# Kernel tuning notes

Measured on AMD Instinct MI355X. Metric: run time of the kernel, lower is better.

The kernel has to match this reference:

```python
import jax, jax.numpy as jnp
import numpy as np

PERIOD = 24
NUM_ITERATIONS = 2


def _window_size():
    w = max(3, PERIOD // 2)  # 12
    if w % 2 == 0:
        w += 1  # 13
    return w


def moving_average(s, w):
    # s: [N, L]; replicate-pad by w//2 on each side, then width-w mean conv ('VALID')
    pad = w // 2
    sp = jnp.pad(s, ((0, 0), (pad, pad)), mode='edge')[:, None, :]  # [N,1,L+2*pad]
    k = jnp.ones((1, 1, w), s.dtype) / w
    y = jax.lax.conv_general_dilated(sp, k, window_strides=(1,), padding='VALID',
                                     dimension_numbers=('NCH', 'OIH', 'NCH'))
    return y[:, 0, :]  # [N, L]


def extract_seasonal(d):
    # d: [N, L] with L a multiple of PERIOD. Strided indices i, i+P, ... correspond
    # to reshape [N, C, P] with fixed last axis; median over cycles, broadcast back.
    N, L = d.shape
    C = L // PERIOD
    sub = d.reshape(N, C, PERIOD)
    med = jnp.median(sub, axis=1)  # [N, P] (C=121 is odd -> matches torch.median)
    return jnp.broadcast_to(med[:, None, :], (N, C, PERIOD)).reshape(N, L)


def setup_inputs() -> dict:
    key = jax.random.key(0)
    x = jax.random.normal(key, (64, 2904, 207), dtype=jnp.float32)
    return {"x": x}


def reference(x):
    # x: [B, L, F] -> process all features at once as [B*F, L]
    B, L, F = x.shape
    s = jnp.transpose(x, (0, 2, 1)).reshape(B * F, L)
    w = _window_size()
    trend = moving_average(s, w)
    for _ in range(NUM_ITERATIONS):
        seasonal = extract_seasonal(s - trend)
        trend = moving_average(s - seasonal, w)
    residual = s - trend - seasonal

    def unflatten(a):
        return jnp.transpose(a.reshape(B, F, L), (0, 2, 1))  # [B, L, F]

    return unflatten(trend), unflatten(seasonal), unflatten(residual)
```

## Files before the change

### kernel.cpp

```cpp
#include <hip/hip_runtime.h>

#define LROW    2904
#define PERIOD  24
#define CYC     121
#define NF      207
#define KF      208
#define NB      64
#define NROWS   13248
#define NSLOT   61
#define NT      256
#define LTILE   24
#define NLT     121
#define K2GRID  (NB * NLT)
#define K2CHUNK (K2GRID / 8)
#define R13     (1.f / 13.f)

typedef unsigned short us2 __attribute__((ext_vector_type(2)));

__device__ __forceinline__ int clampi(int i) {
    return i < 0 ? 0 : (i >= LROW ? LROW - 1 : i);
}
__device__ __forceinline__ unsigned quantk(float d) {
    int ki = (int)fmaf(d, 4096.f, 32768.f);
    ki = ki < 0 ? 0 : (ki > 65535 ? 65535 : ki);
    return (unsigned)ki;
}
__device__ __forceinline__ float dqmid(unsigned k) {
    return ((float)(int)k - 32767.5f) * (1.f / 4096.f);
}

__device__ __forceinline__ unsigned selN(const unsigned (&K)[NSLOT], int thr) {
    unsigned T = 0;
    const us2 one2 = __builtin_bit_cast(us2, 0x00010001u);
    for (int bit = 15; bit >= 0; --bit) {
        unsigned Tp = T | (1u << bit);
        unsigned tm32 = (Tp - 1u) | ((Tp - 1u) << 16);
        us2 tm2 = __builtin_bit_cast(us2, tm32);
        us2 acc = __builtin_bit_cast(us2, 0u);
        #pragma unroll
        for (int s = 0; s < NSLOT; ++s) {
            us2 kv = __builtin_bit_cast(us2, K[s]);
            us2 dd = __builtin_elementwise_sub_sat(kv, tm2);
            us2 mm = __builtin_elementwise_min(dd, one2);
            acc = acc + mm;
        }
        unsigned a = __builtin_bit_cast(unsigned, acc);
        int cnt = (int)(a & 0xFFFFu) + (int)(a >> 16);
        if (cnt >= thr) T = Tp;
    }
    return T;
}

__global__ __launch_bounds__(256) void k_keys(const float* __restrict__ x,
                                              unsigned* __restrict__ keys) {
    __shared__ float T[62 * NF];
    const int b  = blockIdx.x;
    const int cp = blockIdx.y;
    const int fl = threadIdx.x;
    const int fe = fl < NF ? fl : NF - 1;
    const int l0 = cp * 48;
    const float* xb = x + (size_t)b * (LROW * NF);
    unsigned* kb = keys + ((size_t)b * PERIOD * NSLOT + cp) * KF + fl;

    if (cp != 0 && cp != 60) {
        const float2* s2 = (const float2*)(xb + (size_t)(l0 - 8) * NF);
        float2* t2 = (float2*)T;
        for (int i = fl; i < 62 * NF / 2; i += NT) t2[i] = s2[i];
    } else {
        for (int i = fl; i < 62 * NF; i += NT) {
            int lr = i / NF, ff = i - lr * NF;
            T[i] = xb[(size_t)clampi(l0 - 8 + lr) * NF + ff];
        }
    }
    __syncthreads();

    float r[13];
    #pragma unroll
    for (int i = 0; i < 13; ++i) r[i] = T[(i + 1) * NF + fe];
    float sum = ((r[0]+r[1])+(r[2]+r[3]))+((r[4]+r[5])+(r[6]+r[7]))
              + ((r[8]+r[9])+(r[10]+r[11])) + r[12];

    if (cp < 60) {
        unsigned pend[PERIOD];
        #pragma unroll
        for (int j = 0; j < 48; ++j) {
            float xn = T[(j + 14) * NF + fe];
            sum += xn - r[0];
            unsigned k = quantk(r[7] - sum * R13);
            if (j < 24) pend[j] = k;
            else if (fl < KF)
                kb[(size_t)(j - 24) * (NSLOT * KF)] = pend[j - 24] | (k << 16);
            #pragma unroll
            for (int i = 0; i < 12; ++i) r[i] = r[i + 1];
            r[12] = xn;
        }
    } else {
        #pragma unroll
        for (int j = 0; j < 24; ++j) {
            float xn = T[(j + 14) * NF + fe];
            sum += xn - r[0];
            unsigned k = quantk(r[7] - sum * R13);
            if (fl < KF)
                kb[(size_t)j * (NSLOT * KF)] = k | 0xFFFF0000u;
            #pragma unroll
            for (int i = 0; i < 12; ++i) r[i] = r[i + 1];
            r[12] = xn;
        }
    }
}

__global__ __launch_bounds__(256) void k_med0(const unsigned* __restrict__ keys,
                                              unsigned short* __restrict__ m0key) {
    const int d  = blockIdx.x;
    const int bp = (d & 7) * 192 + (d >> 3);
    const int fl = threadIdx.x;
    const int fx = fl < KF ? fl : KF - 1;
    unsigned K[NSLOT];
    const unsigned* kp = keys + (size_t)bp * NSLOT * KF + fx;
    #pragma unroll
    for (int s = 0; s < NSLOT; ++s) K[s] = kp[(size_t)s * KF];
    unsigned T = selN(K, 62);
    if (fl < KF) m0key[(size_t)bp * KF + fl] = (unsigned short)T;
}

__global__ __launch_bounds__(256) void k_edge2(const unsigned* __restrict__ keys,
                                               const unsigned short* __restrict__ m0key,
                                               float* __restrict__ medBedge) {
    const int d  = blockIdx.x;
    const int be = (d & 7) * 96 + (d >> 3);
    const int b = be / 12, e = be - 12 * b;
    const int p = (e < 6) ? e : e + 12;
    const int fl = threadIdx.x;
    const int fx = fl < KF ? fl : KF - 1;

    float m0[PERIOD];
    #pragma unroll
    for (int q = 0; q < PERIOD; ++q)
        m0[q] = dqmid(m0key[(size_t)(b * PERIOD + q) * KF + fx]);

    float wph = 0.f, we = 0.f;
    #pragma unroll
    for (int ee = 0; ee < 12; ++ee) if (ee == e) {
        const int pp = (ee < 6) ? ee : ee + 12;
        #pragma unroll
        for (int t = 0; t < 13; ++t) wph += m0[(pp + 18 + t) % 24];
        #pragma unroll
        for (int t = -6; t <= 6; ++t) {
            int aa = pp + t; if (aa < 0) aa = 0; if (aa > 23) aa = 23;
            we += m0[aa];
        }
    }

    unsigned K[NSLOT];
    const unsigned* kp = keys + (size_t)(b * PERIOD + p) * NSLOT * KF + fx;
    #pragma unroll
    for (int s = 0; s < NSLOT; ++s) K[s] = kp[(size_t)s * KF];

    unsigned m = (unsigned)m0key[(size_t)(b * PERIOD + p) * KF + fx];
    unsigned xk = ((p < 6) ? K[0] : K[60]) & 0xFFFFu;
    unsigned y = quantk(dqmid(xk) + (we - wph) * R13);

    int thr = (y > m) ? 61 : 63;
    unsigned v = selN(K, thr);
    bool up = (y > m) && (xk <= m);
    bool dn = (y < m) && (xk >= m);
    unsigned nm = up ? (y < v ? y : v) : (dn ? (y > v ? y : v) : m);
    if (fl < KF)
        medBedge[(size_t)(b * 12 + e) * KF + fl] = dqmid(nm) + wph * R13;
}

__global__ __launch_bounds__(NT, 5) void stl_outputs(const float* __restrict__ x,
                                                     const unsigned short* __restrict__ m0key,
                                                     const float* __restrict__ medBedge,
                                                     float* __restrict__ out) {
    __shared__ float T[(LTILE + 12) * NF];

    const int d   = blockIdx.x;
    const int blk = (d & 7) * K2CHUNK + (d >> 3);
    const int b  = blk / NLT;
    const int kk = blk - b * NLT;
    const int l0 = kk * LTILE;
    const int t  = threadIdx.x;
    const float* xb = x + (size_t)b * (LROW * NF);

    if (kk != 0 && kk != NLT - 1) {
        const float2* s2 = (const float2*)(xb + (size_t)(l0 - 6) * NF);
        float2* t2 = (float2*)T;
        for (int i = t; i < (LTILE + 12) * NF / 2; i += NT) t2[i] = s2[i];
    } else {
        for (int i = t; i < (LTILE + 12) * NF; i += NT) {
            int lr = i / NF;
            int ff = i - lr * NF;
            T[i] = xb[(size_t)clampi(l0 - 6 + lr) * NF + ff];
        }
    }
    __syncthreads();

    if (t < NF) {
        float m0[PERIOD];
        #pragma unroll
        for (int q = 0; q < PERIOD; ++q)
            m0[q] = dqmid(m0key[(size_t)(b * PERIOD + q) * KF + t]);
        float W0[PERIOD];
        {
            float s = 0.f;
            #pragma unroll
            for (int q = 0; q < 13; ++q) s += m0[q];
            W0[0] = s;
            #pragma unroll
            for (int q = 1; q < PERIOD; ++q)
                W0[q] = W0[q - 1] + m0[(q + 12) % 24] - m0[q - 1];
        }
        float lm[PERIOD];
        #pragma unroll
        for (int e = 0; e < 12; ++e) {
            int p = (e < 6) ? e : e + 12;
            lm[p] = medBedge[(size_t)(b * 12 + e) * KF + t];
        }
        #pragma unroll
        for (int p = 6; p < 18; ++p) lm[p] = m0[p] + W0[p - 6] * R13;
        float wt[PERIOD];
        {
            float s = 0.f;
            #pragma unroll
            for (int q = 0; q < 13; ++q) s += lm[q];
            wt[0] = s;
            #pragma unroll
            for (int q = 1; q < PERIOD; ++q)
                wt[q] = wt[q - 1] + lm[(q + 12) % 24] - lm[q - 1];
        }

        float s13 = 0.f;
        #pragma unroll
        for (int r = 0; r < 13; ++r) s13 += T[r * NF + t];

        const bool edgeLo = (kk == 0), edgeHi = (kk == NLT - 1);
        const size_t S = (size_t)NROWS * LROW;
        const size_t obase = (size_t)b * (LROW * NF) + (size_t)l0 * NF + (size_t)t;

        #pragma unroll
        for (int j = 0; j < LTILE; ++j) {
            float W = wt[(j + 18) % 24];
            if (edgeLo && j < 6) {
                float w = 0.f;
                #pragma unroll
                for (int jj = -6; jj <= 6; ++jj) { int m = j + jj; if (m < 0) m = 0; w += lm[m]; }
                W = w;
            }
            if (edgeHi && j >= 18) {
                float w = 0.f;
                #pragma unroll
                for (int jj = -6; jj <= 6; ++jj) { int m = j + jj; if (m > 23) m = 23; w += lm[m]; }
                W = w;
            }
            float tr = (s13 - W) * R13;
            float se = lm[j];
            float re = T[(j + 6) * NF + t] - tr - se;
            size_t o = obase + (size_t)(j * NF);
            __builtin_nontemporal_store(tr, &out[o]);
            __builtin_nontemporal_store(se, &out[S + o]);
            __builtin_nontemporal_store(re, &out[2 * S + o]);
            if (j < LTILE - 1)
                s13 += T[(j + 13) * NF + t] - T[j * NF + t];
        }
    }
}

extern "C" void kernel_launch(void* const* d_in, const int* in_sizes, int n_in,
                              void* d_out, int out_size, void* d_ws, size_t ws_size,
                              hipStream_t stream) {
    const float* x = (const float*)d_in[0];
    float* out = (float*)d_out;
    float* wsf = (float*)d_ws;
    (void)in_sizes; (void)n_in; (void)out_size; (void)ws_size;

    unsigned*       keys     = (unsigned*)wsf;
    unsigned short* m0key    = (unsigned short*)(wsf + 19489792);
    float*          medBedge = wsf + 19489792 + 159744;

    hipLaunchKernelGGL(k_keys,   dim3(NB, NSLOT), dim3(NT), 0, stream, x, keys);
    hipLaunchKernelGGL(k_med0,   dim3(NB * PERIOD), dim3(NT), 0, stream, keys, m0key);
    hipLaunchKernelGGL(k_edge2,  dim3(NB * 12), dim3(NT), 0, stream, keys, m0key, medBedge);
    hipLaunchKernelGGL(stl_outputs, dim3(K2GRID), dim3(NT), 0, stream,
                       x, m0key, medBedge, out);
}
```

Measured before the change: 336.9 us.

## Split median selection across thread pairs and use nontemporal key stores

```diff
diff --git a/kernel.cpp b/kernel.cpp
--- a/kernel.cpp
+++ b/kernel.cpp
@@ -29,7 +29,7 @@
     return ((float)(int)k - 32767.5f) * (1.f / 4096.f);
 }
 
-__device__ __forceinline__ unsigned selN(const unsigned (&K)[NSLOT], int thr) {
+__device__ __forceinline__ unsigned selN_split(const unsigned (&K)[31], int thr) {
     unsigned T = 0;
     const us2 one2 = __builtin_bit_cast(us2, 0x00010001u);
     for (int bit = 15; bit >= 0; --bit) {
@@ -38,7 +38,7 @@
         us2 tm2 = __builtin_bit_cast(us2, tm32);
         us2 acc = __builtin_bit_cast(us2, 0u);
         #pragma unroll
-        for (int s = 0; s < NSLOT; ++s) {
+        for (int s = 0; s < 31; ++s) {
             us2 kv = __builtin_bit_cast(us2, K[s]);
             us2 dd = __builtin_elementwise_sub_sat(kv, tm2);
             us2 mm = __builtin_elementwise_min(dd, one2);
@@ -46,6 +46,7 @@
         }
         unsigned a = __builtin_bit_cast(unsigned, acc);
         int cnt = (int)(a & 0xFFFFu) + (int)(a >> 16);
+        cnt += __shfl_xor(cnt, 1);
         if (cnt >= thr) T = Tp;
     }
     return T;
@@ -89,7 +90,8 @@
             unsigned k = quantk(r[7] - sum * R13);
             if (j < 24) pend[j] = k;
             else if (fl < KF)
-                kb[(size_t)(j - 24) * (NSLOT * KF)] = pend[j - 24] | (k << 16);
+                __builtin_nontemporal_store(pend[j - 24] | (k << 16),
+                                            &kb[(size_t)(j - 24) * (NSLOT * KF)]);
             #pragma unroll
             for (int i = 0; i < 12; ++i) r[i] = r[i + 1];
             r[12] = xn;
@@ -101,7 +103,8 @@
             sum += xn - r[0];
             unsigned k = quantk(r[7] - sum * R13);
             if (fl < KF)
-                kb[(size_t)j * (NSLOT * KF)] = k | 0xFFFF0000u;
+                __builtin_nontemporal_store(k | 0xFFFF0000u,
+                                            &kb[(size_t)j * (NSLOT * KF)]);
             #pragma unroll
             for (int i = 0; i < 12; ++i) r[i] = r[i + 1];
             r[12] = xn;
@@ -113,14 +116,21 @@
                                               unsigned short* __restrict__ m0key) {
     const int d  = blockIdx.x;
     const int bp = (d & 7) * 192 + (d >> 3);
-    const int fl = threadIdx.x;
-    const int fx = fl < KF ? fl : KF - 1;
-    unsigned K[NSLOT];
-    const unsigned* kp = keys + (size_t)bp * NSLOT * KF + fx;
-    #pragma unroll
-    for (int s = 0; s < NSLOT; ++s) K[s] = kp[(size_t)s * KF];
-    unsigned T = selN(K, 62);
-    if (fl < KF) m0key[(size_t)bp * KF + fl] = (unsigned short)T;
+    const int fb = blockIdx.y;
+    const int t  = threadIdx.x;
+    const int f  = fb * 128 + (t >> 1);
+    const int half = t & 1;
+    const int fx = f < KF ? f : KF - 1;
+
+    const unsigned* kp = keys + (size_t)bp * (NSLOT * KF) + fx
+                       + (half ? (size_t)30 * KF : 0);
+    unsigned K[31];
+    #pragma unroll
+    for (int s = 0; s < 31; ++s) K[s] = kp[(size_t)s * KF];
+    if (!half) K[30] = 0;
+
+    unsigned T = selN_split(K, 62);
+    if (!half && f < KF) m0key[(size_t)bp * KF + f] = (unsigned short)T;
 }
 
 __global__ __launch_bounds__(256) void k_edge2(const unsigned* __restrict__ keys,
@@ -130,8 +140,11 @@
     const int be = (d & 7) * 96 + (d >> 3);
     const int b = be / 12, e = be - 12 * b;
     const int p = (e < 6) ? e : e + 12;
-    const int fl = threadIdx.x;
-    const int fx = fl < KF ? fl : KF - 1;
+    const int fb = blockIdx.y;
+    const int t  = threadIdx.x;
+    const int f  = fb * 128 + (t >> 1);
+    const int half = t & 1;
+    const int fx = f < KF ? f : KF - 1;
 
     float m0[PERIOD];
     #pragma unroll
@@ -143,30 +156,33 @@
     for (int ee = 0; ee < 12; ++ee) if (ee == e) {
         const int pp = (ee < 6) ? ee : ee + 12;
         #pragma unroll
-        for (int t = 0; t < 13; ++t) wph += m0[(pp + 18 + t) % 24];
-        #pragma unroll
-        for (int t = -6; t <= 6; ++t) {
-            int aa = pp + t; if (aa < 0) aa = 0; if (aa > 23) aa = 23;
+        for (int q = 0; q < 13; ++q) wph += m0[(pp + 18 + q) % 24];
+        #pragma unroll
+        for (int q = -6; q <= 6; ++q) {
+            int aa = pp + q; if (aa < 0) aa = 0; if (aa > 23) aa = 23;
             we += m0[aa];
         }
     }
 
-    unsigned K[NSLOT];
-    const unsigned* kp = keys + (size_t)(b * PERIOD + p) * NSLOT * KF + fx;
-    #pragma unroll
-    for (int s = 0; s < NSLOT; ++s) K[s] = kp[(size_t)s * KF];
+    const unsigned* kp = keys + (size_t)(b * PERIOD + p) * (NSLOT * KF) + fx
+                       + (half ? (size_t)30 * KF : 0);
+    unsigned K[31];
+    #pragma unroll
+    for (int s = 0; s < 31; ++s) K[s] = kp[(size_t)s * KF];
+    if (!half) K[30] = 0;
 
     unsigned m = (unsigned)m0key[(size_t)(b * PERIOD + p) * KF + fx];
-    unsigned xk = ((p < 6) ? K[0] : K[60]) & 0xFFFFu;
+    unsigned xk = keys[(size_t)(b * PERIOD + p) * (NSLOT * KF)
+                       + (size_t)(p < 6 ? 0 : 60) * KF + fx] & 0xFFFFu;
     unsigned y = quantk(dqmid(xk) + (we - wph) * R13);
 
     int thr = (y > m) ? 61 : 63;
-    unsigned v = selN(K, thr);
+    unsigned v = selN_split(K, thr);
     bool up = (y > m) && (xk <= m);
     bool dn = (y < m) && (xk >= m);
     unsigned nm = up ? (y < v ? y : v) : (dn ? (y > v ? y : v) : m);
-    if (fl < KF)
-        medBedge[(size_t)(b * 12 + e) * KF + fl] = dqmid(nm) + wph * R13;
+    if (!half && f < KF)
+        medBedge[(size_t)(b * 12 + e) * KF + f] = dqmid(nm) + wph * R13;
 }
 
 __global__ __launch_bounds__(NT, 5) void stl_outputs(const float* __restrict__ x,
@@ -279,8 +295,8 @@
     float*          medBedge = wsf + 19489792 + 159744;
 
     hipLaunchKernelGGL(k_keys,   dim3(NB, NSLOT), dim3(NT), 0, stream, x, keys);
-    hipLaunchKernelGGL(k_med0,   dim3(NB * PERIOD), dim3(NT), 0, stream, keys, m0key);
-    hipLaunchKernelGGL(k_edge2,  dim3(NB * 12), dim3(NT), 0, stream, keys, m0key, medBedge);
+    hipLaunchKernelGGL(k_med0,   dim3(NB * PERIOD, 2), dim3(NT), 0, stream, keys, m0key);
+    hipLaunchKernelGGL(k_edge2,  dim3(NB * 12, 2), dim3(NT), 0, stream, keys, m0key, medBedge);
     hipLaunchKernelGGL(stl_outputs, dim3(K2GRID), dim3(NT), 0, stream,
                        x, m0key, medBedge, out);
 }
```

Result: no change. 335.2 us, median of 2 (-0.5%).
